# Kernel optimization log

Hardware: AMD Instinct MI355X
Metric: run time of the kernel (lower is better)

## Reference

```python
import jax, jax.numpy as jnp
import numpy as np

B, L, D = 64, 512, 768

def setup_inputs() -> dict:
    key = jax.random.key(0)
    k1, k2, k3, k4 = jax.random.split(key, 4)
    hidden_states = jax.random.normal(k1, (B, L, D), dtype=jnp.float32)
    # nn.Linear(hidden_size, hidden_size): weight [D, D], bias [D]
    W = jax.random.normal(k2, (D, D), dtype=jnp.float32) * (1.0 / np.sqrt(D))
    b = jax.random.normal(k3, (D,), dtype=jnp.float32) * 0.02
    # context_vector: [D, 1]
    context_vector = jax.random.normal(k4, (D, 1), dtype=jnp.float32)
    return {"hidden_states": hidden_states, "W": W, "b": b, "context_vector": context_vector}

def reference(hidden_states, W, b, context_vector):
    # tanh(dense(h)): [B, L, D]; torch Linear uses x @ W.T + b
    proj = jnp.tanh(jnp.einsum('bld,ed->ble', hidden_states, W) + b)
    # scores: [B, L]
    scores = jnp.einsum('bld,d->bl', proj, context_vector[:, 0])
    # softmax over sequence dim (dim=1)
    attention_weights = jax.nn.softmax(scores, axis=1)
    # weighted sum over sequence: [B, D]
    weighted_output = jnp.einsum('bld,bl->bd', hidden_states, attention_weights)
    return (weighted_output, attention_weights)
```

## Files before the change

kernel.cpp:

```cpp
#include <hip/hip_runtime.h>
#include <hip/hip_bf16.h>


using half8 = __attribute__((ext_vector_type(8))) _Float16;
using f32x4 = __attribute__((ext_vector_type(4))) float;

#define AS1 __attribute__((address_space(1)))
#define AS3 __attribute__((address_space(3)))

__device__ __forceinline__ void gload_lds16(const void* g, void* l) {
  __builtin_amdgcn_global_load_lds((const AS1 void*)g, (AS3 void*)l, 16, 0, 0);
}

__device__ __forceinline__ unsigned short f2h(float x) {
  _Float16 h = (_Float16)x;
  return __builtin_bit_cast(unsigned short, h);
}

__device__ __forceinline__ float tanh_fast(float x) {
  return 1.0f - __fdividef(2.0f, 1.0f + __expf(2.0f * x));
}


__global__ void convert_h(const float4* __restrict__ H4, ushort4* __restrict__ Ah) {
  int i = blockIdx.x * 256 + threadIdx.x;
  float4 x = H4[i];
  ushort4 o;
  o.x = f2h(x.x); o.y = f2h(x.y); o.z = f2h(x.z); o.w = f2h(x.w);
  Ah[i] = o;
}

__global__ void convert_w(const float4* __restrict__ W4, ushort4* __restrict__ Wt) {
  int i = blockIdx.x * 256 + threadIdx.x;
  float4 x = W4[i];
  ushort4 o;
  o.x = f2h(x.x); o.y = f2h(x.y); o.z = f2h(x.z); o.w = f2h(x.w);
  Wt[i] = o;
}

__global__ __launch_bounds__(256) void gemm_scores(
    const ushort* __restrict__ Ah, const ushort* __restrict__ Wt,
    const float* __restrict__ bias, const float* __restrict__ cvec,
    float* __restrict__ part) {
  __shared__ ushort ldsA[2][4096];
  __shared__ ushort ldsB[2][4096];
  __shared__ float scpart[2][128];

  const int tid = threadIdx.x;
  const int lane = tid & 63;
  const int wid = tid >> 6;
  const int wr = wid >> 1, wc = wid & 1;
  const int m = lane & 15, q = lane >> 4;

  const int bid = blockIdx.x;
  const int xcd = bid & 7;
  const int slot = bid >> 3;
  const int mtile = xcd * 32 + slot / 6;
  const int ntile = slot % 6;

  const char* const Abase = (const char*)Ah + (size_t)(mtile * 128) * 1536;
  const char* const Bbase = (const char*)Wt + (size_t)(ntile * 128) * 1536;

  const int up = (tid & 7) ^ ((tid >> 3) & 7);
  const int lr_s = tid >> 3;
  const size_t src0 = (size_t)((up >> 2) * 64 + lr_s) * 1536 + (up & 3) * 16;
  const size_t src1 = (size_t)((up >> 2) * 64 + 32 + lr_s) * 1536 + (up & 3) * 16;
  const int wavebase = wid << 10;

  f32x4 acc[4][4];
  #pragma unroll
  for (int i = 0; i < 4; ++i)
    #pragma unroll
    for (int j = 0; j < 4; ++j)
      acc[i][j] = (f32x4){0.f, 0.f, 0.f, 0.f};

  auto stage = [&](int kt, int s) {
    gload_lds16(Abase + src0 + kt * 64, (char*)ldsA[s] + wavebase);
    gload_lds16(Abase + src1 + kt * 64, (char*)ldsA[s] + 4096 + wavebase);
    gload_lds16(Bbase + src0 + kt * 64, (char*)ldsB[s] + wavebase);
    gload_lds16(Bbase + src1 + kt * 64, (char*)ldsB[s] + 4096 + wavebase);
  };

  const int aslot = ((wr * 4 + q) ^ (m & 7)) * 16;
  const int bslot = ((wc * 4 + q) ^ (m & 7)) * 16;

  auto compute = [&](int s) {
    const char* Ab = (const char*)ldsA[s];
    const char* Bb = (const char*)ldsB[s];
    half8 areg[4], breg[4];
    #pragma unroll
    for (int mi = 0; mi < 4; ++mi)
      areg[mi] = *(const half8*)(Ab + (mi * 16 + m) * 128 + aslot);
    #pragma unroll
    for (int ni = 0; ni < 4; ++ni)
      breg[ni] = *(const half8*)(Bb + (ni * 16 + m) * 128 + bslot);
    #pragma unroll
    for (int mi = 0; mi < 4; ++mi)
      #pragma unroll
      for (int ni = 0; ni < 4; ++ni)
        acc[mi][ni] = __builtin_amdgcn_mfma_f32_16x16x32_f16(
            areg[mi], breg[ni], acc[mi][ni], 0, 0, 0);
  };

  stage(0, 0);
  __syncthreads();
  #pragma unroll
  for (int kb2 = 0; kb2 < 12; ++kb2) {
    stage(2 * kb2 + 1, 1);
    compute(0);
    __syncthreads();
    if (kb2 < 11) stage(2 * kb2 + 2, 0);
    compute(1);
    __syncthreads();
  }

  float bb[4], cc[4];
  #pragma unroll
  for (int ni = 0; ni < 4; ++ni) {
    int e = ntile * 128 + wc * 64 + ni * 16 + m;
    bb[ni] = bias[e];
    cc[ni] = cvec[e];
  }
  #pragma unroll
  for (int mi = 0; mi < 4; ++mi) {
    #pragma unroll
    for (int j = 0; j < 4; ++j) {
      float s = 0.f;
      #pragma unroll
      for (int ni = 0; ni < 4; ++ni)
        s += tanh_fast(acc[mi][ni][j] + bb[ni]) * cc[ni];
      s += __shfl_xor(s, 1);
      s += __shfl_xor(s, 2);
      s += __shfl_xor(s, 4);
      s += __shfl_xor(s, 8);
      if (m == 0) scpart[wc][wr * 64 + mi * 16 + q * 4 + j] = s;
    }
  }
  __syncthreads();
  if (tid < 128)
    part[ntile * 32768 + mtile * 128 + tid] = scpart[0][tid] + scpart[1][tid];
}

__global__ void wsum_fused(const ushort* __restrict__ Ah, const float* __restrict__ prt,
                           float* __restrict__ out) {
  int b = blockIdx.x, dc = blockIdx.y;
  int t = threadIdx.x;
  __shared__ float w[512];
  __shared__ float redm[2], reds[2];

  float s[4];
  #pragma unroll
  for (int i = 0; i < 4; ++i) {
    int r = b * 512 + t + i * 128;
    s[i] = prt[r] + prt[32768 + r] + prt[2 * 32768 + r] +
           prt[3 * 32768 + r] + prt[4 * 32768 + r] + prt[5 * 32768 + r];
  }
  float mx = fmaxf(fmaxf(s[0], s[1]), fmaxf(s[2], s[3]));
  #pragma unroll
  for (int o = 32; o >= 1; o >>= 1) mx = fmaxf(mx, __shfl_xor(mx, o));
  if ((t & 63) == 0) redm[t >> 6] = mx;
  __syncthreads();
  mx = fmaxf(redm[0], redm[1]);

  float e[4], sm = 0.f;
  #pragma unroll
  for (int i = 0; i < 4; ++i) { e[i] = __expf(s[i] - mx); sm += e[i]; }
  #pragma unroll
  for (int o = 32; o >= 1; o >>= 1) sm += __shfl_xor(sm, o);
  if ((t & 63) == 0) reds[t >> 6] = sm;
  __syncthreads();
  float inv = 1.0f / (reds[0] + reds[1]);
  #pragma unroll
  for (int i = 0; i < 4; ++i) w[t + i * 128] = e[i] * inv;
  __syncthreads();

  int d0 = dc * 256 + t * 2;
  const ushort* hp = Ah + (size_t)b * 512 * 768 + d0;
  float a0 = 0.f, a1 = 0.f;
  #pragma unroll 8
  for (int l = 0; l < 512; ++l) {
    unsigned u = *(const unsigned*)(hp + (size_t)l * 768);
    float wl = w[l];
    a0 += wl * (float)__builtin_bit_cast(_Float16, (unsigned short)(u & 0xffff));
    a1 += wl * (float)__builtin_bit_cast(_Float16, (unsigned short)(u >> 16));
  }
  out[b * 768 + d0] = a0;
  out[b * 768 + d0 + 1] = a1;

  if (dc == 0) {
    #pragma unroll
    for (int i = 0; i < 4; ++i)
      out[49152 + b * 512 + t + i * 128] = w[t + i * 128];
  }
}

extern "C" void kernel_launch(void* const* d_in, const int* in_sizes, int n_in,
                              void* d_out, int out_size, void* d_ws, size_t ws_size,
                              hipStream_t stream) {
  const float* H    = (const float*)d_in[0];
  const float* W    = (const float*)d_in[1];
  const float* bias = (const float*)d_in[2];
  const float* cvec = (const float*)d_in[3];
  float* out = (float*)d_out;

  char* ws = (char*)d_ws;
  ushort* Ah = (ushort*)(ws + 0);
  ushort* Wt = (ushort*)(ws + 50331648);
  float*  prt = (float*)(ws + 51511296);

  hipLaunchKernelGGL(convert_h, dim3(24576), dim3(256), 0, stream,
                     (const float4*)H, (ushort4*)Ah);
  hipLaunchKernelGGL(convert_w, dim3(576), dim3(256), 0, stream,
                     (const float4*)W, (ushort4*)Wt);
  hipLaunchKernelGGL(gemm_scores, dim3(1536), dim3(256), 0, stream,
                     Ah, Wt, bias, cvec, prt);
  hipLaunchKernelGGL(wsum_fused, dim3(64, 3), dim3(128), 0, stream,
                     Ah, prt, out);
}
```

Measured before the change: 112.5 us.

## Fuse fp32-to-fp16 conversion of hidden states into GEMM A-tile staging

Removes the separate convert_h pass over the full hidden-state tensor. The GEMM now reads fp32 rows directly into registers, converts them to fp16 and writes them into swizzled LDS, prefetching one K-step ahead. The weighted-sum kernel reads the fp32 input directly, which also improves its accuracy. The cost is that the GEMM now reads twice as many A bytes (each A tile is re-read by 6 N-tiles) and loses the async global-to-LDS path for A. It also does more VALU and register work per iteration.

```diff
diff --git a/kernel.cpp b/kernel.cpp
--- a/kernel.cpp
+++ b/kernel.cpp
@@ -19,15 +19,6 @@
 
 __device__ __forceinline__ float tanh_fast(float x) {
   return 1.0f - __fdividef(2.0f, 1.0f + __expf(2.0f * x));
-}
-
-
-__global__ void convert_h(const float4* __restrict__ H4, ushort4* __restrict__ Ah) {
-  int i = blockIdx.x * 256 + threadIdx.x;
-  float4 x = H4[i];
-  ushort4 o;
-  o.x = f2h(x.x); o.y = f2h(x.y); o.z = f2h(x.z); o.w = f2h(x.w);
-  Ah[i] = o;
 }
 
 __global__ void convert_w(const float4* __restrict__ W4, ushort4* __restrict__ Wt) {
@@ -39,7 +30,7 @@
 }
 
 __global__ __launch_bounds__(256) void gemm_scores(
-    const ushort* __restrict__ Ah, const ushort* __restrict__ Wt,
+    const float* __restrict__ H, const ushort* __restrict__ Wt,
     const float* __restrict__ bias, const float* __restrict__ cvec,
     float* __restrict__ part) {
   __shared__ ushort ldsA[2][4096];
@@ -58,7 +49,6 @@
   const int mtile = xcd * 32 + slot / 6;
   const int ntile = slot % 6;
 
-  const char* const Abase = (const char*)Ah + (size_t)(mtile * 128) * 1536;
   const char* const Bbase = (const char*)Wt + (size_t)(ntile * 128) * 1536;
 
   const int up = (tid & 7) ^ ((tid >> 3) & 7);
@@ -67,6 +57,13 @@
   const size_t src1 = (size_t)((up >> 2) * 64 + 32 + lr_s) * 1536 + (up & 3) * 16;
   const int wavebase = wid << 10;
 
+  const int arow = tid >> 1, kh = tid & 1;
+  const float4* const asrc =
+      (const float4*)(H + (size_t)(mtile * 128 + arow) * 768) + kh * 4;
+  const int a_lr = arow & 63, a_half = arow >> 6;
+  const int wbyte0 = a_lr * 128 + (((a_half * 4 + kh * 2 + 0) ^ (a_lr & 7)) << 4);
+  const int wbyte1 = a_lr * 128 + (((a_half * 4 + kh * 2 + 1) ^ (a_lr & 7)) << 4);
+
   f32x4 acc[4][4];
   #pragma unroll
   for (int i = 0; i < 4; ++i)
@@ -74,43 +71,57 @@
     for (int j = 0; j < 4; ++j)
       acc[i][j] = (f32x4){0.f, 0.f, 0.f, 0.f};
 
-  auto stage = [&](int kt, int s) {
-    gload_lds16(Abase + src0 + kt * 64, (char*)ldsA[s] + wavebase);
-    gload_lds16(Abase + src1 + kt * 64, (char*)ldsA[s] + 4096 + wavebase);
-    gload_lds16(Bbase + src0 + kt * 64, (char*)ldsB[s] + wavebase);
-    gload_lds16(Bbase + src1 + kt * 64, (char*)ldsB[s] + 4096 + wavebase);
-  };
-
   const int aslot = ((wr * 4 + q) ^ (m & 7)) * 16;
   const int bslot = ((wc * 4 + q) ^ (m & 7)) * 16;
 
-  auto compute = [&](int s) {
-    const char* Ab = (const char*)ldsA[s];
-    const char* Bb = (const char*)ldsB[s];
-    half8 areg[4], breg[4];
-    #pragma unroll
-    for (int mi = 0; mi < 4; ++mi)
-      areg[mi] = *(const half8*)(Ab + (mi * 16 + m) * 128 + aslot);
-    #pragma unroll
-    for (int ni = 0; ni < 4; ++ni)
-      breg[ni] = *(const half8*)(Bb + (ni * 16 + m) * 128 + bslot);
-    #pragma unroll
-    for (int mi = 0; mi < 4; ++mi)
+  auto cvt8 = [](float4 u, float4 v) -> half8 {
+    half8 r;
+    r[0] = (_Float16)u.x; r[1] = (_Float16)u.y;
+    r[2] = (_Float16)u.z; r[3] = (_Float16)u.w;
+    r[4] = (_Float16)v.x; r[5] = (_Float16)v.y;
+    r[6] = (_Float16)v.z; r[7] = (_Float16)v.w;
+    return r;
+  };
+
+  float4 a_in[4];
+  #pragma unroll
+  for (int c = 0; c < 4; ++c) a_in[c] = asrc[c];
+  gload_lds16(Bbase + src0, (char*)ldsB[0] + wavebase);
+  gload_lds16(Bbase + src1, (char*)ldsB[0] + 4096 + wavebase);
+  *(half8*)((char*)ldsA[0] + wbyte0) = cvt8(a_in[0], a_in[1]);
+  *(half8*)((char*)ldsA[0] + wbyte1) = cvt8(a_in[2], a_in[3]);
+  __syncthreads();
+
+  #pragma unroll
+  for (int t = 0; t < 24; ++t) {
+    const int cur = t & 1, nxt = cur ^ 1;
+    if (t < 23) {
+      #pragma unroll
+      for (int c = 0; c < 4; ++c) a_in[c] = asrc[(t + 1) * 8 + c];
+      gload_lds16(Bbase + src0 + (t + 1) * 64, (char*)ldsB[nxt] + wavebase);
+      gload_lds16(Bbase + src1 + (t + 1) * 64, (char*)ldsB[nxt] + 4096 + wavebase);
+    }
+    {
+      const char* Ab = (const char*)ldsA[cur];
+      const char* Bb = (const char*)ldsB[cur];
+      half8 areg[4], breg[4];
+      #pragma unroll
+      for (int mi = 0; mi < 4; ++mi)
+        areg[mi] = *(const half8*)(Ab + (mi * 16 + m) * 128 + aslot);
       #pragma unroll
       for (int ni = 0; ni < 4; ++ni)
-        acc[mi][ni] = __builtin_amdgcn_mfma_f32_16x16x32_f16(
-            areg[mi], breg[ni], acc[mi][ni], 0, 0, 0);
-  };
-
-  stage(0, 0);
-  __syncthreads();
-  #pragma unroll
-  for (int kb2 = 0; kb2 < 12; ++kb2) {
-    stage(2 * kb2 + 1, 1);
-    compute(0);
-    __syncthreads();
-    if (kb2 < 11) stage(2 * kb2 + 2, 0);
-    compute(1);
+        breg[ni] = *(const half8*)(Bb + (ni * 16 + m) * 128 + bslot);
+      #pragma unroll
+      for (int mi = 0; mi < 4; ++mi)
+        #pragma unroll
+        for (int ni = 0; ni < 4; ++ni)
+          acc[mi][ni] = __builtin_amdgcn_mfma_f32_16x16x32_f16(
+              areg[mi], breg[ni], acc[mi][ni], 0, 0, 0);
+    }
+    if (t < 23) {
+      *(half8*)((char*)ldsA[nxt] + wbyte0) = cvt8(a_in[0], a_in[1]);
+      *(half8*)((char*)ldsA[nxt] + wbyte1) = cvt8(a_in[2], a_in[3]);
+    }
     __syncthreads();
   }
 
@@ -141,7 +152,7 @@
     part[ntile * 32768 + mtile * 128 + tid] = scpart[0][tid] + scpart[1][tid];
 }
 
-__global__ void wsum_fused(const ushort* __restrict__ Ah, const float* __restrict__ prt,
+__global__ void wsum_fused(const float* __restrict__ H, const float* __restrict__ prt,
                            float* __restrict__ out) {
   int b = blockIdx.x, dc = blockIdx.y;
   int t = threadIdx.x;
@@ -175,14 +186,14 @@
   __syncthreads();
 
   int d0 = dc * 256 + t * 2;
-  const ushort* hp = Ah + (size_t)b * 512 * 768 + d0;
+  const float2* hp = (const float2*)(H + (size_t)b * 512 * 768 + d0);
   float a0 = 0.f, a1 = 0.f;
   #pragma unroll 8
   for (int l = 0; l < 512; ++l) {
-    unsigned u = *(const unsigned*)(hp + (size_t)l * 768);
+    float2 u = hp[(size_t)l * 384];
     float wl = w[l];
-    a0 += wl * (float)__builtin_bit_cast(_Float16, (unsigned short)(u & 0xffff));
-    a1 += wl * (float)__builtin_bit_cast(_Float16, (unsigned short)(u >> 16));
+    a0 += wl * u.x;
+    a1 += wl * u.y;
   }
   out[b * 768 + d0] = a0;
   out[b * 768 + d0 + 1] = a1;
@@ -204,16 +215,13 @@
   float* out = (float*)d_out;
 
   char* ws = (char*)d_ws;
-  ushort* Ah = (ushort*)(ws + 0);
-  ushort* Wt = (ushort*)(ws + 50331648);
-  float*  prt = (float*)(ws + 51511296);
-
-  hipLaunchKernelGGL(convert_h, dim3(24576), dim3(256), 0, stream,
-                     (const float4*)H, (ushort4*)Ah);
+  ushort* Wt = (ushort*)(ws + 0);
+  float*  prt = (float*)(ws + 1179648);
+
   hipLaunchKernelGGL(convert_w, dim3(576), dim3(256), 0, stream,
                      (const float4*)W, (ushort4*)Wt);
   hipLaunchKernelGGL(gemm_scores, dim3(1536), dim3(256), 0, stream,
-                     Ah, Wt, bias, cvec, prt);
+                     H, Wt, bias, cvec, prt);
   hipLaunchKernelGGL(wsum_fused, dim3(64, 3), dim3(128), 0, stream,
-                     Ah, prt, out);
-}
+                     H, prt, out);
+}
```

Result: slower. 114.9 us (+2.2%).
